# Performance work log

Measured on AMD Instinct MI355X. Metric: run time of the kernel, lower is better.

Reference implementation:

```python
import jax, jax.numpy as jnp
import numpy as np

N_NODES = 50000
N_EDGES = 800000
IN_CH = 128
OUT_CH = 64
HEADS = 4


def setup_inputs() -> dict:
    key = jax.random.key(0)
    k1, k2, k3, k4, k5 = jax.random.split(key, 5)
    feature = jax.random.normal(k1, (N_NODES, IN_CH), dtype=jnp.float32)
    edge_index = jax.random.randint(k2, (2, N_EDGES), 0, N_NODES, dtype=jnp.int64)
    lin_w = jax.random.normal(k3, (IN_CH, HEADS * OUT_CH), dtype=jnp.float32) / np.sqrt(IN_CH)
    att_src = jax.random.normal(k4, (HEADS, OUT_CH), dtype=jnp.float32) / np.sqrt(OUT_CH)
    att_dst = jax.random.normal(k5, (HEADS, OUT_CH), dtype=jnp.float32) / np.sqrt(OUT_CH)
    bias = jnp.zeros((OUT_CH,), dtype=jnp.float32)
    return {"feature": feature, "edge_index": edge_index, "lin_w": lin_w,
            "att_src": att_src, "att_dst": att_dst, "bias": bias}


def _gat(feature, src, dst, lin_w, att_src, att_dst, bias):
    N = feature.shape[0]
    H, C = att_src.shape
    # linear projection -> [N, H, C]
    x = (feature @ lin_w).reshape(N, H, C)
    # per-node attention logits [N, H]
    a_src = jnp.einsum('nhc,hc->nh', x, att_src)
    a_dst = jnp.einsum('nhc,hc->nh', x, att_dst)
    # per-edge logits, LeakyReLU (negative_slope=0.2 as in PyG GATConv)
    alpha = jax.nn.leaky_relu(a_src[src] + a_dst[dst], negative_slope=0.2)  # [E, H]
    # segment softmax over destination neighborhoods (self-loops guarantee non-empty)
    amax = jax.ops.segment_max(alpha, dst, num_segments=N)[dst]
    ex = jnp.exp(alpha - amax)
    denom = jax.ops.segment_sum(ex, dst, num_segments=N)[dst]
    w = ex / denom  # [E, H]
    # weighted scatter-add of source features
    msg = x[src] * w[:, :, None]  # [E, H, C]
    out = jax.ops.segment_sum(msg, dst, num_segments=N)  # [N, H, C]
    # concat=False -> mean over heads, then bias
    return out.mean(axis=1) + bias


def reference(feature, edge_index, lin_w, att_src, att_dst, bias):
    N = feature.shape[0]
    loop = jnp.arange(N, dtype=edge_index.dtype)
    src = jnp.concatenate([edge_index[0], loop])  # add_self_loops=True default
    dst = jnp.concatenate([edge_index[1], loop])
    return _gat(feature, src, dst, lin_w, att_src, att_dst, bias)
```

## Files before the change

kernel.cpp:

```cpp
#include <hip/hip_runtime.h>
#include <hip/hip_fp16.h>

typedef _Float16 f16x8 __attribute__((ext_vector_type(8)));
typedef _Float16 f16x4 __attribute__((ext_vector_type(4)));
typedef float    f32x4 __attribute__((ext_vector_type(4)));

constexpr int NN  = 50000;
constexpr int NE  = 800000;
constexpr int IC  = 128;
constexpr int HC  = 256;
constexpr int OC  = 64;
constexpr int CAP = 64;

__global__ __launch_bounds__(256) void fillprep(
    const float* __restrict__ w, __half* __restrict__ wt,
    const int* __restrict__ ei, int* __restrict__ cnt,
    unsigned short* __restrict__ csrsrc)
{
    if (blockIdx.x < IC) {
        const int k = blockIdx.x;
        const int m = threadIdx.x;
        wt[m * IC + k] = __float2half(w[k * HC + m]);
        return;
    }
    const int e = (blockIdx.x - IC) * 256 + threadIdx.x;
    if (e >= NE) return;
    const int s = ei[e];
    const int d = ei[NE + e];
    const int pos = atomicAdd(&cnt[d], 1);
    if (pos < CAP)
        csrsrc[d * CAP + pos] = (unsigned short)s;
}

__global__ __launch_bounds__(256) void proj_mfma(
    const float* __restrict__ feat, const __half* __restrict__ wt,
    const float* __restrict__ att_s, const float* __restrict__ att_d,
    __half* __restrict__ Xh, float* __restrict__ As, float* __restrict__ Ad)
{
    __shared__ _Float16 smem[64 * 260];
    _Float16* sf = smem;
    _Float16* so = smem;
    const int t  = threadIdx.x;
    const int w  = t >> 6;
    const int l  = t & 63;
    const int n0 = blockIdx.x * 64;

    {
        const int r  = t >> 2;
        const int gr = min(n0 + r, NN - 1);
        const float* src = feat + (size_t)gr * IC + (t & 3) * 32;
#pragma unroll
        for (int i = 0; i < 4; ++i) {
            const float4 f0 = *reinterpret_cast<const float4*>(src + i * 8);
            const float4 f1 = *reinterpret_cast<const float4*>(src + i * 8 + 4);
            f16x8 hv;
            hv[0] = (_Float16)f0.x; hv[1] = (_Float16)f0.y;
            hv[2] = (_Float16)f0.z; hv[3] = (_Float16)f0.w;
            hv[4] = (_Float16)f1.x; hv[5] = (_Float16)f1.y;
            hv[6] = (_Float16)f1.z; hv[7] = (_Float16)f1.w;
            const int cc = (t & 3) * 4 + i;
            *reinterpret_cast<f16x8*>(&sf[(r * 16 + (cc ^ (r & 7))) * 8]) = hv;
        }
    }
    __syncthreads();

    const int lhi = l >> 4, llo = l & 15;
    f32x4 acc[4][4] = {};

#pragma unroll
    for (int ks = 0; ks < 4; ++ks) {
        f16x8 a[4], b[4];
#pragma unroll
        for (int mg = 0; mg < 4; ++mg) {
            const int row = w * 64 + mg * 16 + llo;
            a[mg] = *reinterpret_cast<const f16x8*>(
                wt + (size_t)row * IC + ks * 32 + lhi * 8);
        }
#pragma unroll
        for (int ng = 0; ng < 4; ++ng) {
            const int rr = ng * 16 + llo;
            const int cc = ks * 4 + lhi;
            b[ng] = *reinterpret_cast<const f16x8*>(
                &sf[(rr * 16 + (cc ^ (rr & 7))) * 8]);
        }
#pragma unroll
        for (int mg = 0; mg < 4; ++mg)
#pragma unroll
            for (int ng = 0; ng < 4; ++ng)
                acc[mg][ng] = __builtin_amdgcn_mfma_f32_16x16x32_f16(
                    a[mg], b[ng], acc[mg][ng], 0, 0, 0);
    }

    float4 avs[4], avd[4];
#pragma unroll
    for (int mg = 0; mg < 4; ++mg) {
        const int ch = w * 64 + mg * 16 + 4 * lhi;
        avs[mg] = *reinterpret_cast<const float4*>(att_s + ch);
        avd[mg] = *reinterpret_cast<const float4*>(att_d + ch);
    }
    __syncthreads();

#pragma unroll
    for (int ng = 0; ng < 4; ++ng) {
        const int n = n0 + ng * 16 + llo;
        float ps = 0.f, pd = 0.f;
#pragma unroll
        for (int mg = 0; mg < 4; ++mg) {
            const f32x4 v = acc[mg][ng];
            ps += v[0] * avs[mg].x + v[1] * avs[mg].y
                + v[2] * avs[mg].z + v[3] * avs[mg].w;
            pd += v[0] * avd[mg].x + v[1] * avd[mg].y
                + v[2] * avd[mg].z + v[3] * avd[mg].w;
            f16x4 pk;
            pk[0] = (_Float16)v[0]; pk[1] = (_Float16)v[1];
            pk[2] = (_Float16)v[2]; pk[3] = (_Float16)v[3];
            *reinterpret_cast<f16x4*>(
                &so[(ng * 16 + llo) * 260 + w * 64 + mg * 16 + 4 * lhi]) = pk;
        }
        ps += __shfl_xor(ps, 16); ps += __shfl_xor(ps, 32);
        pd += __shfl_xor(pd, 16); pd += __shfl_xor(pd, 32);
        if (lhi == 0 && n < NN) {
            As[n * 4 + w] = ps;
            Ad[n * 4 + w] = pd;
        }
    }
    __syncthreads();

#pragma unroll
    for (int rr = 0; rr < 8; ++rr) {
        const int r = w * 16 + rr * 2 + (l >> 5);
        const int n = n0 + r;
        if (n < NN)
            *reinterpret_cast<f16x8*>(&Xh[(size_t)n * HC + 8 * (l & 31)]) =
                *reinterpret_cast<const f16x8*>(&so[r * 260 + 8 * (l & 31)]);
    }
}

__global__ __launch_bounds__(256) void gather_kernel(
    const int* __restrict__ cnt, const unsigned short* __restrict__ csr_src,
    const float* __restrict__ As, const float* __restrict__ Ad,
    const __half* __restrict__ Xh, const float* __restrict__ bias,
    float* __restrict__ out)
{
    const int gid  = blockIdx.x * 256 + threadIdx.x;
    const int w    = gid >> 6;
    const int lane = gid & 63;
    if (w >= NN) return;

    const int deg = min(cnt[w], CAP);
    const int beg = w * CAP;
    const int end = beg + deg;
    const int h   = lane >> 4;

    const float adh = Ad[w * 4 + h];
    float4 acc;
    float den;

    {
        float lg = As[w * 4 + h] + adh;
        lg = lg > 0.f ? lg : 0.2f * lg;
        const float ex = __expf(lg);
        den = ex;
        const float2 xw = *reinterpret_cast<const float2*>(
            Xh + (size_t)w * HC + 4 * lane);
        const __half2* p = reinterpret_cast<const __half2*>(&xw);
        const float2 lo = __half22float2(p[0]);
        const float2 hi = __half22float2(p[1]);
        acc.x = ex * lo.x; acc.y = ex * lo.y;
        acc.z = ex * hi.x; acc.w = ex * hi.y;
    }

    for (int j = beg; j < end; j += 4) {
        int s[4]; float a[4]; float2 x[4];
#pragma unroll
        for (int i = 0; i < 4; ++i) {
            const int jj = j + i;
            s[i] = csr_src[jj < end ? jj : end - 1];
        }
#pragma unroll
        for (int i = 0; i < 4; ++i) a[i] = As[s[i] * 4 + h];
#pragma unroll
        for (int i = 0; i < 4; ++i)
            x[i] = *reinterpret_cast<const float2*>(
                Xh + (size_t)s[i] * HC + 4 * lane);
#pragma unroll
        for (int i = 0; i < 4; ++i) {
            float lg = a[i] + adh;
            lg = lg > 0.f ? lg : 0.2f * lg;
            const float ex = (i == 0 || j + i < end) ? __expf(lg) : 0.f;
            den += ex;
            const __half2* p = reinterpret_cast<const __half2*>(&x[i]);
            const float2 lo = __half22float2(p[0]);
            const float2 hi = __half22float2(p[1]);
            acc.x = fmaf(ex, lo.x, acc.x); acc.y = fmaf(ex, lo.y, acc.y);
            acc.z = fmaf(ex, hi.x, acc.z); acc.w = fmaf(ex, hi.y, acc.w);
        }
    }

    const float inv = 0.25f * __frcp_rn(den);
    acc.x *= inv; acc.y *= inv; acc.z *= inv; acc.w *= inv;

    acc.x += __shfl_xor(acc.x, 16); acc.x += __shfl_xor(acc.x, 32);
    acc.y += __shfl_xor(acc.y, 16); acc.y += __shfl_xor(acc.y, 32);
    acc.z += __shfl_xor(acc.z, 16); acc.z += __shfl_xor(acc.z, 32);
    acc.w += __shfl_xor(acc.w, 16); acc.w += __shfl_xor(acc.w, 32);

    if (lane < 16) {
        const float4 b = *reinterpret_cast<const float4*>(&bias[4 * lane]);
        float4 o;
        o.x = acc.x + b.x; o.y = acc.y + b.y;
        o.z = acc.z + b.z; o.w = acc.w + b.w;
        *reinterpret_cast<float4*>(&out[(size_t)w * OC + 4 * lane]) = o;
    }
}

extern "C" void kernel_launch(void* const* d_in, const int* in_sizes, int n_in,
                              void* d_out, int out_size, void* d_ws, size_t ws_size,
                              hipStream_t stream)
{
    const float* feat = (const float*)d_in[0];
    const int*   ei   = (const int*)d_in[1];
    const float* lw   = (const float*)d_in[2];
    const float* as   = (const float*)d_in[3];
    const float* ad   = (const float*)d_in[4];
    const float* bias = (const float*)d_in[5];
    float* out = (float*)d_out;

    char* ws = (char*)d_ws;
    __half* Xh     = (__half*)ws;          ws += (size_t)NN * HC * 2;
    __half* Wt     = (__half*)ws;          ws += (size_t)HC * IC * 2;
    float*  Asrc   = (float*)ws;           ws += (size_t)NN * 4 * 4;
    float*  Adst   = (float*)ws;           ws += (size_t)NN * 4 * 4;
    int*    cnt    = (int*)ws;             ws += (size_t)NN * 4;
    unsigned short* csrsrc = (unsigned short*)ws;
    ws += (size_t)NN * CAP * 2;

    (void)hipMemsetAsync(cnt, 0, sizeof(int) * (size_t)NN, stream);

    fillprep<<<IC + (NE + 255) / 256, 256, 0, stream>>>(lw, Wt, ei, cnt, csrsrc);
    proj_mfma<<<(NN + 63) / 64, 256, 0, stream>>>(feat, Wt, as, ad, Xh, Asrc, Adst);
    gather_kernel<<<(NN * 64 + 255) / 256, 256, 0, stream>>>(
        cnt, csrsrc, Asrc, Adst, Xh, bias, out);
}
```

Before: 146.1 us.

## Split projected features into channel-quarter planes and gather four edges per wave

The projection now writes features as four separate planes, each holding a 16-channel slice per head, so every plane is 6.4 MB instead of one 25.6 MB array. The gather launches one block per four nodes per quarter and interleaves block indices so that blocks working on the same quarter run together. This is meant to keep each plane's random-access working set cache-resident. Each wave handles four edges at a time with 16 lanes per edge, then reduces across lanes. In exchange, the edge list, attention logits and counts are read four times over, and each lane's load is only 8 bytes.

```diff
diff --git a/kernel.cpp b/kernel.cpp
--- a/kernel.cpp
+++ b/kernel.cpp
@@ -35,7 +35,7 @@
 __global__ __launch_bounds__(256) void proj_mfma(
     const float* __restrict__ feat, const __half* __restrict__ wt,
     const float* __restrict__ att_s, const float* __restrict__ att_d,
-    __half* __restrict__ Xh, float* __restrict__ As, float* __restrict__ Ad)
+    __half* __restrict__ Xq, float* __restrict__ As, float* __restrict__ Ad)
 {
     __shared__ _Float16 smem[64 * 260];
     _Float16* sf = smem;
@@ -126,91 +126,102 @@
     }
     __syncthreads();
 
-#pragma unroll
-    for (int rr = 0; rr < 8; ++rr) {
-        const int r = w * 16 + rr * 2 + (l >> 5);
-        const int n = n0 + r;
-        if (n < NN)
-            *reinterpret_cast<f16x8*>(&Xh[(size_t)n * HC + 8 * (l & 31)]) =
-                *reinterpret_cast<const f16x8*>(&so[r * 260 + 8 * (l & 31)]);
+    {
+        const int q  = l >> 4;
+        const int k  = l & 15;
+        const int hh = k >> 2;
+        const int cc = (k & 3) * 4;
+#pragma unroll
+        for (int rr = 0; rr < 16; ++rr) {
+            const int r = w * 16 + rr;
+            const int n = n0 + r;
+            if (n < NN)
+                *reinterpret_cast<f16x4*>(
+                    &Xq[((size_t)q * NN + n) * 64 + hh * 16 + cc]) =
+                    *reinterpret_cast<const f16x4*>(
+                        &so[r * 260 + hh * 64 + q * 16 + cc]);
+        }
     }
 }
 
 __global__ __launch_bounds__(256) void gather_kernel(
     const int* __restrict__ cnt, const unsigned short* __restrict__ csr_src,
     const float* __restrict__ As, const float* __restrict__ Ad,
-    const __half* __restrict__ Xh, const float* __restrict__ bias,
+    const __half* __restrict__ Xq, const float* __restrict__ bias,
     float* __restrict__ out)
 {
-    const int gid  = blockIdx.x * 256 + threadIdx.x;
-    const int w    = gid >> 6;
-    const int lane = gid & 63;
-    if (w >= NN) return;
+    const int b   = blockIdx.x;
+    const int t   = threadIdx.x;
+    const int wid = t >> 6;
+    const int l   = t & 63;
+    const int q   = (b & 7) >> 1;
+    const int m   = ((b >> 3) << 1) | (b & 1);
+    const int w   = m * 4 + wid;
+
+    const int i4 = l >> 4;
+    const int h  = (l >> 2) & 3;
+    const int c4 = l & 3;
 
     const int deg = min(cnt[w], CAP);
     const int beg = w * CAP;
-    const int end = beg + deg;
-    const int h   = lane >> 4;
-
     const float adh = Ad[w * 4 + h];
-    float4 acc;
-    float den;
+    const __half* xq = Xq + (size_t)q * NN * 64;
+
+    float4 acc = {0.f, 0.f, 0.f, 0.f};
+    float den = 0.f;
+
+    for (int j = 0; j < deg; j += 4) {
+        const int jj = j + i4;
+        const int s  = csr_src[beg + (jj < deg ? jj : deg - 1)];
+        const float a = As[s * 4 + h];
+        const float2 xv = *reinterpret_cast<const float2*>(
+            xq + (size_t)s * 64 + h * 16 + c4 * 4);
+        float lg = a + adh;
+        lg = lg > 0.f ? lg : 0.2f * lg;
+        const float ex = (jj < deg) ? __expf(lg) : 0.f;
+        den += ex;
+        const __half2* p = reinterpret_cast<const __half2*>(&xv);
+        const float2 lo = __half22float2(p[0]);
+        const float2 hi = __half22float2(p[1]);
+        acc.x = fmaf(ex, lo.x, acc.x); acc.y = fmaf(ex, lo.y, acc.y);
+        acc.z = fmaf(ex, hi.x, acc.z); acc.w = fmaf(ex, hi.y, acc.w);
+    }
+
+    acc.x += __shfl_xor(acc.x, 16); acc.x += __shfl_xor(acc.x, 32);
+    acc.y += __shfl_xor(acc.y, 16); acc.y += __shfl_xor(acc.y, 32);
+    acc.z += __shfl_xor(acc.z, 16); acc.z += __shfl_xor(acc.z, 32);
+    acc.w += __shfl_xor(acc.w, 16); acc.w += __shfl_xor(acc.w, 32);
+    den   += __shfl_xor(den, 16);   den   += __shfl_xor(den, 32);
 
     {
         float lg = As[w * 4 + h] + adh;
         lg = lg > 0.f ? lg : 0.2f * lg;
         const float ex = __expf(lg);
-        den = ex;
+        den += ex;
         const float2 xw = *reinterpret_cast<const float2*>(
-            Xh + (size_t)w * HC + 4 * lane);
+            xq + (size_t)w * 64 + h * 16 + c4 * 4);
         const __half2* p = reinterpret_cast<const __half2*>(&xw);
         const float2 lo = __half22float2(p[0]);
         const float2 hi = __half22float2(p[1]);
-        acc.x = ex * lo.x; acc.y = ex * lo.y;
-        acc.z = ex * hi.x; acc.w = ex * hi.y;
-    }
-
-    for (int j = beg; j < end; j += 4) {
-        int s[4]; float a[4]; float2 x[4];
-#pragma unroll
-        for (int i = 0; i < 4; ++i) {
-            const int jj = j + i;
-            s[i] = csr_src[jj < end ? jj : end - 1];
-        }
-#pragma unroll
-        for (int i = 0; i < 4; ++i) a[i] = As[s[i] * 4 + h];
-#pragma unroll
-        for (int i = 0; i < 4; ++i)
-            x[i] = *reinterpret_cast<const float2*>(
-                Xh + (size_t)s[i] * HC + 4 * lane);
-#pragma unroll
-        for (int i = 0; i < 4; ++i) {
-            float lg = a[i] + adh;
-            lg = lg > 0.f ? lg : 0.2f * lg;
-            const float ex = (i == 0 || j + i < end) ? __expf(lg) : 0.f;
-            den += ex;
-            const __half2* p = reinterpret_cast<const __half2*>(&x[i]);
-            const float2 lo = __half22float2(p[0]);
-            const float2 hi = __half22float2(p[1]);
-            acc.x = fmaf(ex, lo.x, acc.x); acc.y = fmaf(ex, lo.y, acc.y);
-            acc.z = fmaf(ex, hi.x, acc.z); acc.w = fmaf(ex, hi.y, acc.w);
-        }
+        acc.x = fmaf(ex, lo.x, acc.x); acc.y = fmaf(ex, lo.y, acc.y);
+        acc.z = fmaf(ex, hi.x, acc.z); acc.w = fmaf(ex, hi.y, acc.w);
     }
 
     const float inv = 0.25f * __frcp_rn(den);
     acc.x *= inv; acc.y *= inv; acc.z *= inv; acc.w *= inv;
 
-    acc.x += __shfl_xor(acc.x, 16); acc.x += __shfl_xor(acc.x, 32);
-    acc.y += __shfl_xor(acc.y, 16); acc.y += __shfl_xor(acc.y, 32);
-    acc.z += __shfl_xor(acc.z, 16); acc.z += __shfl_xor(acc.z, 32);
-    acc.w += __shfl_xor(acc.w, 16); acc.w += __shfl_xor(acc.w, 32);
-
-    if (lane < 16) {
-        const float4 b = *reinterpret_cast<const float4*>(&bias[4 * lane]);
+    acc.x += __shfl_xor(acc.x, 4); acc.x += __shfl_xor(acc.x, 8);
+    acc.y += __shfl_xor(acc.y, 4); acc.y += __shfl_xor(acc.y, 8);
+    acc.z += __shfl_xor(acc.z, 4); acc.z += __shfl_xor(acc.z, 8);
+    acc.w += __shfl_xor(acc.w, 4); acc.w += __shfl_xor(acc.w, 8);
+
+    if (l < 4) {
+        const float4 bq = *reinterpret_cast<const float4*>(
+            &bias[q * 16 + 4 * l]);
         float4 o;
-        o.x = acc.x + b.x; o.y = acc.y + b.y;
-        o.z = acc.z + b.z; o.w = acc.w + b.w;
-        *reinterpret_cast<float4*>(&out[(size_t)w * OC + 4 * lane]) = o;
+        o.x = acc.x + bq.x; o.y = acc.y + bq.y;
+        o.z = acc.z + bq.z; o.w = acc.w + bq.w;
+        *reinterpret_cast<float4*>(&out[(size_t)w * OC + q * 16 + 4 * l]) = o;
     }
 }
 
@@ -227,7 +238,7 @@
     float* out = (float*)d_out;
 
     char* ws = (char*)d_ws;
-    __half* Xh     = (__half*)ws;          ws += (size_t)NN * HC * 2;
+    __half* Xq     = (__half*)ws;          ws += (size_t)NN * HC * 2;
     __half* Wt     = (__half*)ws;          ws += (size_t)HC * IC * 2;
     float*  Asrc   = (float*)ws;           ws += (size_t)NN * 4 * 4;
     float*  Adst   = (float*)ws;           ws += (size_t)NN * 4 * 4;
@@ -238,7 +249,6 @@
     (void)hipMemsetAsync(cnt, 0, sizeof(int) * (size_t)NN, stream);
 
     fillprep<<<IC + (NE + 255) / 256, 256, 0, stream>>>(lw, Wt, ei, cnt, csrsrc);
-    proj_mfma<<<(NN + 63) / 64, 256, 0, stream>>>(feat, Wt, as, ad, Xh, Asrc, Adst);
-    gather_kernel<<<(NN * 64 + 255) / 256, 256, 0, stream>>>(
-        cnt, csrsrc, Asrc, Adst, Xh, bias, out);
-}
+    proj_mfma<<<(NN + 63) / 64, 256, 0, stream>>>(feat, Wt, as, ad, Xq, Asrc, Adst);
+    gather_kernel<<<NN, 256, 0, stream>>>(cnt, csrsrc, Asrc, Adst, Xq, bias, out);
+}
```

Measured after the change: 209.9 us. +43.7%, slower.

## Split edge bucketing into eight sub-buckets by block to reduce atomic contention

Applied to the files above, without the earlier changes.

Edge insertion now scatters into eight per-block-slot sub-buckets, each with its own counters, instead of one shared counter per destination. This spreads atomics across more addresses. A new merge kernel then prefix-sums the sub-counts and compacts them into the per-node bucket that the gather kernel reads. The cost is an extra kernel launch, a larger memset and extra memory traffic. Because each sub-bucket holds at most 16 entries, a node that gets more than 16 edges from one slot drops them, which changes correctness limits on skewed inputs.

```diff
diff --git a/kernel.cpp b/kernel.cpp
--- a/kernel.cpp
+++ b/kernel.cpp
@@ -5,17 +5,18 @@
 typedef _Float16 f16x4 __attribute__((ext_vector_type(4)));
 typedef float    f32x4 __attribute__((ext_vector_type(4)));
 
-constexpr int NN  = 50000;
-constexpr int NE  = 800000;
-constexpr int IC  = 128;
-constexpr int HC  = 256;
-constexpr int OC  = 64;
-constexpr int CAP = 64;
+constexpr int NN   = 50000;
+constexpr int NE   = 800000;
+constexpr int IC   = 128;
+constexpr int HC   = 256;
+constexpr int OC   = 64;
+constexpr int CAP  = 64;
+constexpr int CAPS = 16;
 
 __global__ __launch_bounds__(256) void fillprep(
     const float* __restrict__ w, __half* __restrict__ wt,
-    const int* __restrict__ ei, int* __restrict__ cnt,
-    unsigned short* __restrict__ csrsrc)
+    const int* __restrict__ ei, int* __restrict__ cnt8,
+    unsigned short* __restrict__ sub)
 {
     if (blockIdx.x < IC) {
         const int k = blockIdx.x;
@@ -25,11 +26,41 @@
     }
     const int e = (blockIdx.x - IC) * 256 + threadIdx.x;
     if (e >= NE) return;
+    const int x = blockIdx.x & 7;
     const int s = ei[e];
     const int d = ei[NE + e];
-    const int pos = atomicAdd(&cnt[d], 1);
-    if (pos < CAP)
-        csrsrc[d * CAP + pos] = (unsigned short)s;
+    const int pos = atomicAdd(&cnt8[x * NN + d], 1);
+    if (pos < CAPS)
+        sub[((size_t)x * NN + d) * CAPS + pos] = (unsigned short)s;
+}
+
+__global__ __launch_bounds__(256) void merge_kernel(
+    const int* __restrict__ cnt8, const unsigned short* __restrict__ sub,
+    int* __restrict__ cnt, unsigned short* __restrict__ bucket)
+{
+    const int gid = blockIdx.x * 256 + threadIdx.x;
+    const int w   = gid >> 6;
+    const int l   = gid & 63;
+    if (w >= NN) return;
+
+    int o[9];
+    o[0] = 0;
+#pragma unroll
+    for (int j = 0; j < 8; ++j) {
+        const int c = min(cnt8[j * NN + w], CAPS);
+        o[j + 1] = o[j] + c;
+    }
+    int total = o[8];
+    if (total > CAP) total = CAP;
+    if (l == 0) cnt[w] = total;
+
+    if (l < total) {
+        int j = 0;
+#pragma unroll
+        for (int k = 1; k < 8; ++k) j += (l >= o[k]);
+        bucket[(size_t)w * CAP + l] =
+            sub[((size_t)j * NN + w) * CAPS + (l - o[j])];
+    }
 }
 
 __global__ __launch_bounds__(256) void proj_mfma(
@@ -231,14 +262,18 @@
     __half* Wt     = (__half*)ws;          ws += (size_t)HC * IC * 2;
     float*  Asrc   = (float*)ws;           ws += (size_t)NN * 4 * 4;
     float*  Adst   = (float*)ws;           ws += (size_t)NN * 4 * 4;
+    int*    cnt8   = (int*)ws;             ws += (size_t)8 * NN * 4;
     int*    cnt    = (int*)ws;             ws += (size_t)NN * 4;
-    unsigned short* csrsrc = (unsigned short*)ws;
+    unsigned short* sub    = (unsigned short*)ws;
+    ws += (size_t)8 * NN * CAPS * 2;
+    unsigned short* bucket = (unsigned short*)ws;
     ws += (size_t)NN * CAP * 2;
 
-    (void)hipMemsetAsync(cnt, 0, sizeof(int) * (size_t)NN, stream);
-
-    fillprep<<<IC + (NE + 255) / 256, 256, 0, stream>>>(lw, Wt, ei, cnt, csrsrc);
+    (void)hipMemsetAsync(cnt8, 0, sizeof(int) * (size_t)8 * NN, stream);
+
+    fillprep<<<IC + (NE + 255) / 256, 256, 0, stream>>>(lw, Wt, ei, cnt8, sub);
+    merge_kernel<<<(NN * 64 + 255) / 256, 256, 0, stream>>>(cnt8, sub, cnt, bucket);
     proj_mfma<<<(NN + 63) / 64, 256, 0, stream>>>(feat, Wt, as, ad, Xh, Asrc, Adst);
     gather_kernel<<<(NN * 64 + 255) / 256, 256, 0, stream>>>(
-        cnt, csrsrc, Asrc, Adst, Xh, bias, out);
-}
+        cnt, bucket, Asrc, Adst, Xh, bias, out);
+}
```

New measurement: 142.6 us. 2.4% less time.
